# Performance work log

Measured on AMD Instinct MI355X. Metric: run time of the kernel, lower is better.

The kernel has to match this reference:

```python
import jax, jax.numpy as jnp
import numpy as np

HEADS = 16
DIM_HEAD = 64
QUERY_DIM = 1024
INNER_DIM = HEADS * DIM_HEAD  # 1024
SCALE = DIM_HEAD ** (-0.5)


def setup_inputs() -> dict:
    key = jax.random.key(0)
    ks = jax.random.split(key, 6)
    B, S = 4, 2048
    hidden_states = jax.random.normal(ks[0], (B, S, QUERY_DIM), dtype=jnp.float32)
    # Linear weights stored as [in, out] for x @ W convention
    init = 1.0 / np.sqrt(QUERY_DIM)
    Wq = jax.random.uniform(ks[1], (QUERY_DIM, INNER_DIM), jnp.float32, -init, init)
    Wk = jax.random.uniform(ks[2], (QUERY_DIM, INNER_DIM), jnp.float32, -init, init)
    Wv = jax.random.uniform(ks[3], (QUERY_DIM, INNER_DIM), jnp.float32, -init, init)
    Wo = jax.random.uniform(ks[4], (INNER_DIM, QUERY_DIM), jnp.float32, -init, init)
    bo = jax.random.uniform(ks[5], (QUERY_DIM,), jnp.float32, -init, init)
    return {"hidden_states": hidden_states, "Wq": Wq, "Wk": Wk, "Wv": Wv, "Wo": Wo, "bo": bo}


def reference(hidden_states, Wq, Wk, Wv, Wo, bo):
    B, S, _ = hidden_states.shape
    # Projections
    q = hidden_states @ Wq  # [B,S,inner]
    k = hidden_states @ Wk
    v = hidden_states @ Wv
    # [B, H, S, D]
    q = q.reshape(B, S, HEADS, DIM_HEAD).transpose(0, 2, 1, 3)
    k = k.reshape(B, S, HEADS, DIM_HEAD).transpose(0, 2, 1, 3)
    v = v.reshape(B, S, HEADS, DIM_HEAD).transpose(0, 2, 1, 3)
    # Attention scores and softmax (scale after matmul, as in source)
    scores = jnp.einsum('bhqd,bhkd->bhqk', q, k) * SCALE
    attn = jax.nn.softmax(scores, axis=-1)
    out = jnp.einsum('bhqk,bhkd->bhqd', attn, v)  # [B,H,S,D]
    out = out.transpose(0, 2, 1, 3).reshape(B, S, INNER_DIM)
    return out @ Wo + bo
```

## Files before the change

### kernel.cpp

```cpp
#include <hip/hip_runtime.h>
#include <stdint.h>

typedef short v8s __attribute__((ext_vector_type(8)));
typedef float v4f __attribute__((ext_vector_type(4)));
typedef unsigned int u32;
typedef unsigned short us;

#define LOG2E 1.44269504088896340736f

__device__ __forceinline__ u32 f2u(float x) {
  union { float f; u32 u; } t; t.f = x; return t.u;
}

__device__ __forceinline__ unsigned short bfr(float x) {
  u32 u = f2u(x);
  u32 r = u + 0x7FFFu + ((u >> 16) & 1u);
  return (unsigned short)(r >> 16);
}

__device__ __forceinline__ u32 pk2(float a, float b) {
  return __builtin_amdgcn_perm(f2u(b) + 0x8000u, f2u(a) + 0x8000u, 0x07060302u);
}

__device__ __forceinline__ void async16(const void* g, void* l) {
  __builtin_amdgcn_global_load_lds(
      (const __attribute__((address_space(1))) u32*)g,
      (__attribute__((address_space(3))) u32*)l, 16, 0, 0);
}

#define MFMA_K32(A, B, C) __builtin_amdgcn_mfma_f32_16x16x32_bf16((A), (B), (C), 0, 0, 0)

__global__ void cast_h_kernel(const float4* __restrict__ in, ushort4* __restrict__ out, int n4) {
  int i = blockIdx.x * blockDim.x + threadIdx.x;
  if (i < n4) {
    float4 v = in[i];
    ushort4 o;
    o.x = bfr(v.x); o.y = bfr(v.y); o.z = bfr(v.z); o.w = bfr(v.w);
    out[i] = o;
  }
}

__global__ void transpose_cast4_kernel(const float* __restrict__ W0, const float* __restrict__ W1,
                                       const float* __restrict__ W2, const float* __restrict__ W3,
                                       us* __restrict__ O0, us* __restrict__ O1,
                                       us* __restrict__ O2, us* __restrict__ O3) {
  __shared__ float tile[32][33];
  const int z = blockIdx.z;
  const float* in = (z == 0) ? W0 : (z == 1) ? W1 : (z == 2) ? W2 : W3;
  us* out = (z == 0) ? O0 : (z == 1) ? O1 : (z == 2) ? O2 : O3;
  const float scale = (z == 0) ? 0.125f * LOG2E : 1.0f;
  const int N = 1024;
  int n0 = blockIdx.x * 32, k0 = blockIdx.y * 32;
  int tx = threadIdx.x, ty = threadIdx.y;
#pragma unroll
  for (int j = 0; j < 32; j += 8)
    tile[ty + j][tx] = in[(size_t)(k0 + ty + j) * N + n0 + tx];
  __syncthreads();
#pragma unroll
  for (int j = 0; j < 32; j += 8)
    out[(size_t)(n0 + ty + j) * 1024 + k0 + tx] = bfr(tile[tx][ty + j] * scale);
}

template <int MODE>
__global__ __launch_bounds__(256)
void gemm_bt_kernel(const us* __restrict__ A, const us* __restrict__ Bt,
                    us* __restrict__ dQ, us* __restrict__ dK, us* __restrict__ dV,
                    float* __restrict__ outF, const float* __restrict__ bias) {
  __shared__ __align__(16) us sm[MODE == 3 ? 16896 : 16384];
  us* As = sm;
  us* Bs = sm + 8192;
  const int tid = threadIdx.x;
  const int wid = tid >> 6;
  const int lane = tid & 63;
  const int quad = lane >> 4;
  const int l16 = lane & 15;
  const int tile_m = blockIdx.y * 128;
  const int tile_n = blockIdx.x * 128;
  const bool vpath = (MODE == 3) && (tile_n >= 2048);

  const int srow = wid * 32 + (lane >> 3);
  const int sc = lane & 7;

  v4f zero = {0.f, 0.f, 0.f, 0.f};
  v4f acc[4][4];
#pragma unroll
  for (int i = 0; i < 4; ++i)
#pragma unroll
    for (int j = 0; j < 4; ++j) acc[i][j] = zero;

  const int wm = (wid >> 1) * 64;
  const int wn = (wid & 1) * 64;

  for (int k0 = 0; k0 < 1024; k0 += 64) {
#pragma unroll
    for (int it = 0; it < 4; ++it) {
      int rr = srow + it * 8;
      int cg = sc ^ (rr & 7);
      async16(A + (size_t)(tile_m + rr) * 1024 + k0 + cg * 8, &As[rr * 64 + sc * 8]);
      async16(Bt + (size_t)(tile_n + rr) * 1024 + k0 + cg * 8, &Bs[rr * 64 + sc * 8]);
    }
    __syncthreads();
#pragma unroll
    for (int ks = 0; ks < 2; ++ks) {
      v8s a[4], b[4];
#pragma unroll
      for (int i = 0; i < 4; ++i) {
        int row = wm + i * 16 + l16;
        a[i] = *(const v8s*)&As[row * 64 + (((ks * 4 + quad) ^ (row & 7)) * 8)];
      }
#pragma unroll
      for (int j = 0; j < 4; ++j) {
        int row = wn + j * 16 + l16;
        b[j] = *(const v8s*)&Bs[row * 64 + (((ks * 4 + quad) ^ (row & 7)) * 8)];
      }
      if (vpath) {
#pragma unroll
        for (int i = 0; i < 4; ++i)
#pragma unroll
          for (int j = 0; j < 4; ++j)
            acc[i][j] = MFMA_K32(a[i], b[j], acc[i][j]);
      } else {
#pragma unroll
        for (int i = 0; i < 4; ++i)
#pragma unroll
          for (int j = 0; j < 4; ++j)
            acc[i][j] = MFMA_K32(b[j], a[i], acc[i][j]);
      }
    }
    __syncthreads();
  }

  if (MODE == 2) {
#pragma unroll
    for (int i = 0; i < 4; ++i) {
      int row = tile_m + wm + i * 16 + l16;
#pragma unroll
      for (int j = 0; j < 4; ++j) {
        int col = tile_n + wn + j * 16 + quad * 4;
        float4 bv = *(const float4*)&bias[col];
        float4 o;
        o.x = acc[i][j][0] + bv.x; o.y = acc[i][j][1] + bv.y;
        o.z = acc[i][j][2] + bv.z; o.w = acc[i][j][3] + bv.w;
        *(float4*)&outF[(size_t)row * 1024 + col] = o;
      }
    }
  } else if (!vpath) {
    us* base = (tile_n < 1024) ? dQ : dK;
    const int coln = tile_n & 1023;
#pragma unroll
    for (int i = 0; i < 4; ++i) {
      int row = tile_m + wm + i * 16 + l16;
      int b_ = row >> 11, s_ = row & 2047;
#pragma unroll
      for (int j = 0; j < 4; ++j) {
        int col = coln + wn + j * 16 + quad * 4;
        int h = (col >> 6) & 15, d = col & 63;
        uint2 pk = make_uint2(pk2(acc[i][j][0], acc[i][j][1]), pk2(acc[i][j][2], acc[i][j][3]));
        *(uint2*)&base[((size_t)(b_ * 16 + h) * 2048 + s_) * 64 + d] = pk;
      }
    }
  } else {
    const int vn = tile_n - 2048;
#pragma unroll
    for (int i = 0; i < 4; ++i) {
      int sp = wm + (i >> 1) * 32 + quad * 8 + (i & 1) * 4;
#pragma unroll
      for (int j = 0; j < 4; ++j) {
        int col = wn + j * 16 + l16;
        uint2 pk = make_uint2(pk2(acc[i][j][0], acc[i][j][1]), pk2(acc[i][j][2], acc[i][j][3]));
        *(uint2*)&sm[col * 132 + sp] = pk;
      }
    }
    __syncthreads();
    const int b_ = tile_m >> 11;
    const int sbase = tile_m & 2047;
#pragma unroll
    for (int it = 0; it < 8; ++it) {
      int u = it * 256 + tid;
      int col = u >> 4, sp = (u & 15) * 8;
      v8s val = *(const v8s*)&sm[col * 132 + sp];
      int colg = vn + col;
      int h = (colg >> 6) & 15, d = colg & 63;
      *(v8s*)&dV[((size_t)(b_ * 16 + h) * 64 + d) * 2048 + sbase + sp] = val;
    }
  }
}

__global__ __launch_bounds__(256, 2)
void flash_kernel(const us* __restrict__ Q, const us* __restrict__ K,
                  const us* __restrict__ Vt, us* __restrict__ O) {
  __shared__ __align__(16) us sm[16384];
  us* Ks = sm;
  us* Vts = sm + 8192;

  const int tid = threadIdx.x;
  const int wid = tid >> 6;
  const int lane = tid & 63;
  const int quad = lane >> 4;
  const int l16 = lane & 15;
  const int id = blockIdx.x;
  const int bh = id & 63;
  const int q0 = (id >> 6) * 256;
  const int wq = wid * 64;
  const us* Qp = Q + (size_t)bh * (2048 * 64);
  const us* Kp = K + (size_t)bh * (2048 * 64);
  const us* Vp = Vt + (size_t)bh * (64 * 2048);

  v8s qB[4][2];
#pragma unroll
  for (int mi = 0; mi < 4; ++mi)
#pragma unroll
    for (int ks = 0; ks < 2; ++ks)
      qB[mi][ks] = *(const v8s*)&Qp[(size_t)(q0 + wq + mi * 16 + l16) * 64 + ks * 32 + quad * 8];

  v4f zero = {0.f, 0.f, 0.f, 0.f};
  v4f o[4][4];
#pragma unroll
  for (int i = 0; i < 4; ++i)
#pragma unroll
    for (int mi = 0; mi < 4; ++mi) o[i][mi] = zero;
  v4f l_acc[4] = {zero, zero, zero, zero};
  const us one_bf = 0x3F80;
  const v8s ones = {(short)one_bf, (short)one_bf, (short)one_bf, (short)one_bf,
                    (short)one_bf, (short)one_bf, (short)one_bf, (short)one_bf};

  for (int kv0 = 0; kv0 < 2048; kv0 += 128) {
    __syncthreads();
    {
      int r0 = wid * 32 + (lane >> 3);
      int c = lane & 7;
#pragma unroll
      for (int it = 0; it < 4; ++it) {
        int rr = r0 + it * 8;
        int cg = c ^ (rr & 7);
        async16(Kp + (size_t)(kv0 + rr) * 64 + cg * 8, &Ks[rr * 64 + c * 8]);
      }
    }
    {
      int d0 = wid * 16 + (lane >> 4);
      int c = lane & 15;
#pragma unroll
      for (int it = 0; it < 4; ++it) {
        int dd = d0 + it * 4;
        int cg = c ^ (dd & 15);
        async16(Vp + (size_t)dd * 2048 + kv0 + cg * 8, &Vts[dd * 128 + c * 8]);
      }
    }
    __syncthreads();

#pragma unroll
    for (int hf = 0; hf < 2; ++hf) {
      v4f sT[4][4];
#pragma unroll
      for (int m = 0; m < 4; ++m)
#pragma unroll
        for (int mi = 0; mi < 4; ++mi) sT[m][mi] = zero;
#pragma unroll
      for (int ks = 0; ks < 2; ++ks) {
        v8s kA[4];
#pragma unroll
        for (int m = 0; m < 4; ++m) {
          int kvr = hf * 64 + m * 16 + l16;
          int cc = (ks * 4 + quad) ^ (l16 & 7);
          kA[m] = *(const v8s*)&Ks[kvr * 64 + cc * 8];
        }
#pragma unroll
        for (int m = 0; m < 4; ++m)
#pragma unroll
          for (int mi = 0; mi < 4; ++mi)
            sT[m][mi] = MFMA_K32(kA[m], qB[mi][ks], sT[m][mi]);
      }

#pragma unroll
      for (int cp = 0; cp < 2; ++cp) {
        v8s bp[4];
#pragma unroll
        for (int mi = 0; mi < 4; ++mi) {
          union { u32 w[4]; v8s s; } u;
#pragma unroll
          for (int dm = 0; dm < 2; ++dm) {
            int m = cp * 2 + dm;
            float p0 = __builtin_amdgcn_exp2f(sT[m][mi][0]);
            float p1 = __builtin_amdgcn_exp2f(sT[m][mi][1]);
            float p2 = __builtin_amdgcn_exp2f(sT[m][mi][2]);
            float p3 = __builtin_amdgcn_exp2f(sT[m][mi][3]);
            u.w[dm * 2] = pk2(p0, p1);
            u.w[dm * 2 + 1] = pk2(p2, p3);
          }
          bp[mi] = u.s;
          l_acc[mi] = MFMA_K32(ones, bp[mi], l_acc[mi]);
        }
#pragma unroll
        for (int i = 0; i < 4; ++i) {
          int d = i * 16 + l16;
          int cc = (hf * 8 + cp * 4 + quad) ^ (d & 15);
          v8s vt = *(const v8s*)&Vts[d * 128 + cc * 8];
#pragma unroll
          for (int mi = 0; mi < 4; ++mi)
            o[i][mi] = MFMA_K32(vt, bp[mi], o[i][mi]);
        }
      }
    }
  }

  float invl[4];
#pragma unroll
  for (int mi = 0; mi < 4; ++mi) invl[mi] = 1.0f / l_acc[mi][0];

  __syncthreads();
#pragma unroll
  for (int mi = 0; mi < 4; ++mi) {
    int q = wq + mi * 16 + l16;
#pragma unroll
    for (int i = 0; i < 4; ++i)
#pragma unroll
      for (int rp = 0; rp < 4; rp += 2) {
        int d = i * 16 + quad * 4 + rp;
        u32 pk = pk2(o[i][mi][rp] * invl[mi], o[i][mi][rp + 1] * invl[mi]);
        *(u32*)&sm[q * 64 + ((d >> 3) ^ (q & 7)) * 8 + (d & 7)] = pk;
      }
  }
  __syncthreads();
  const int b_ = bh >> 4, h_ = bh & 15;
#pragma unroll
  for (int it = 0; it < 8; ++it) {
    int u = it * 256 + tid;
    int row = u >> 3, ch = u & 7;
    v8s val = *(const v8s*)&sm[row * 64 + (ch ^ (row & 7)) * 8];
    *(v8s*)&O[((size_t)(b_ * 2048 + q0 + row)) * 1024 + h_ * 64 + ch * 8] = val;
  }
}

extern "C" void kernel_launch(void* const* d_in, const int* in_sizes, int n_in,
                              void* d_out, int out_size, void* d_ws, size_t ws_size,
                              hipStream_t stream) {
  const float* Hs = (const float*)d_in[0];
  const float* Wq = (const float*)d_in[1];
  const float* Wk = (const float*)d_in[2];
  const float* Wv = (const float*)d_in[3];
  const float* Wo = (const float*)d_in[4];
  const float* bo = (const float*)d_in[5];
  float* out = (float*)d_out;
  char* ws = (char*)d_ws;
  const size_t MiB = 1ull << 20;
  us* Hb  = (us*)(ws);
  us* Wqt = (us*)(ws + 16 * MiB);
  us* Wkt = (us*)(ws + 18 * MiB);
  us* Wvt = (us*)(ws + 20 * MiB);
  us* Wot = (us*)(ws + 22 * MiB);
  us* Qb  = (us*)(ws + 24 * MiB);
  us* Kb  = (us*)(ws + 40 * MiB);
  us* Vtb = (us*)(ws + 56 * MiB);
  us* Ob  = Hb;
  (void)Wkt; (void)Wvt;

  cast_h_kernel<<<8192, 256, 0, stream>>>((const float4*)Hs, (ushort4*)Hb, 2097152);
  transpose_cast4_kernel<<<dim3(32, 32, 4), dim3(32, 8), 0, stream>>>(Wq, Wk, Wv, Wo,
                                                                      Wqt, Wkt, Wvt, Wot);
  gemm_bt_kernel<3><<<dim3(24, 64), 256, 0, stream>>>(Hb, Wqt, Qb, Kb, Vtb, nullptr, nullptr);
  flash_kernel<<<512, 256, 0, stream>>>(Qb, Kb, Vtb, Ob);
  gemm_bt_kernel<2><<<dim3(8, 64), 256, 0, stream>>>(Ob, Wot, nullptr, nullptr, nullptr, out, bo);
}
```

Before: 256.0 us.

## Triple-buffer GEMM with async prefetch, 128x256 tiles, and MFMA priority hints

Rewrites the projection GEMM to use 512-thread blocks with 128x256 output tiles. A three-stage LDS ring is fed by async global-to-LDS loads issued two k-steps ahead, with vmcnt waits replacing the double __syncthreads per iteration. It also raises wave priority around MFMA blocks in both the GEMM and the flash attention kernel. The goal is to hide global load latency and improve B-tile reuse, at the cost of 144KB LDS per block (limiting occupancy) and fewer blocks for the small output GEMM (256 blocks).

```diff
diff --git a/kernel.cpp b/kernel.cpp
--- a/kernel.cpp
+++ b/kernel.cpp
@@ -62,24 +62,44 @@
 }
 
 template <int MODE>
-__global__ __launch_bounds__(256)
-void gemm_bt_kernel(const us* __restrict__ A, const us* __restrict__ Bt,
-                    us* __restrict__ dQ, us* __restrict__ dK, us* __restrict__ dV,
-                    float* __restrict__ outF, const float* __restrict__ bias) {
-  __shared__ __align__(16) us sm[MODE == 3 ? 16896 : 16384];
-  us* As = sm;
-  us* Bs = sm + 8192;
+__global__ __launch_bounds__(512, 2)
+void gemm3_kernel(const us* __restrict__ A, const us* __restrict__ Bt,
+                  us* __restrict__ dQ, us* __restrict__ dK, us* __restrict__ dV,
+                  float* __restrict__ outF, const float* __restrict__ bias) {
+  __shared__ __align__(16) us sm[73728];
+  us* const AsB = sm;
+  us* const BsB = sm + 3 * 8192;
+
   const int tid = threadIdx.x;
   const int wid = tid >> 6;
   const int lane = tid & 63;
   const int quad = lane >> 4;
   const int l16 = lane & 15;
   const int tile_m = blockIdx.y * 128;
-  const int tile_n = blockIdx.x * 128;
+  const int tile_n = blockIdx.x * 256;
   const bool vpath = (MODE == 3) && (tile_n >= 2048);
 
-  const int srow = wid * 32 + (lane >> 3);
-  const int sc = lane & 7;
+  const int srow = tid >> 3;
+  const int sc = tid & 7;
+  const int scg = sc ^ (srow & 7);
+
+  const us* const GA = A + (size_t)(tile_m + srow) * 1024 + scg * 8;
+  const us* const GB = Bt + (size_t)(tile_n + srow) * 1024 + scg * 8;
+  us* const LA = AsB + srow * 64 + sc * 8;
+  us* const LB = BsB + srow * 64 + sc * 8;
+
+  auto ISSUE = [&](int j, int b) {
+    const us* ga = GA + j * 64;
+    us* la = LA + b * 8192;
+#pragma unroll
+    for (int it = 0; it < 2; ++it)
+      async16(ga + it * 64 * 1024, la + it * 64 * 64);
+    const us* gb = GB + j * 64;
+    us* lb = LB + b * 16384;
+#pragma unroll
+    for (int it = 0; it < 4; ++it)
+      async16(gb + it * 64 * 1024, lb + it * 64 * 64);
+  };
 
   v4f zero = {0.f, 0.f, 0.f, 0.f};
   v4f acc[4][4];
@@ -88,18 +108,30 @@
 #pragma unroll
     for (int j = 0; j < 4; ++j) acc[i][j] = zero;
 
-  const int wm = (wid >> 1) * 64;
-  const int wn = (wid & 1) * 64;
-
-  for (int k0 = 0; k0 < 1024; k0 += 64) {
-#pragma unroll
-    for (int it = 0; it < 4; ++it) {
-      int rr = srow + it * 8;
-      int cg = sc ^ (rr & 7);
-      async16(A + (size_t)(tile_m + rr) * 1024 + k0 + cg * 8, &As[rr * 64 + sc * 8]);
-      async16(Bt + (size_t)(tile_n + rr) * 1024 + k0 + cg * 8, &Bs[rr * 64 + sc * 8]);
-    }
-    __syncthreads();
+  const int wm = (wid >> 2) * 64;
+  const int wn = (wid & 3) * 64;
+
+  ISSUE(0, 0);
+  ISSUE(1, 1);
+
+  int bt = 0;
+#pragma unroll 1
+  for (int t = 0; t < 16; ++t) {
+    if (t < 15)
+      asm volatile("s_waitcnt vmcnt(6)" ::: "memory");
+    else
+      asm volatile("s_waitcnt vmcnt(0)" ::: "memory");
+    __builtin_amdgcn_s_barrier();
+    asm volatile("" ::: "memory");
+
+    if (t + 2 < 16) {
+      int b2 = bt + 2;
+      if (b2 >= 3) b2 -= 3;
+      ISSUE(t + 2, b2);
+    }
+
+    const us* As = AsB + bt * 8192;
+    const us* Bs = BsB + bt * 16384;
 #pragma unroll
     for (int ks = 0; ks < 2; ++ks) {
       v8s a[4], b[4];
@@ -113,6 +145,7 @@
         int row = wn + j * 16 + l16;
         b[j] = *(const v8s*)&Bs[row * 64 + (((ks * 4 + quad) ^ (row & 7)) * 8)];
       }
+      __builtin_amdgcn_s_setprio(1);
       if (vpath) {
 #pragma unroll
         for (int i = 0; i < 4; ++i)
@@ -126,8 +159,9 @@
           for (int j = 0; j < 4; ++j)
             acc[i][j] = MFMA_K32(b[j], a[i], acc[i][j]);
       }
-    }
-    __syncthreads();
+      __builtin_amdgcn_s_setprio(0);
+    }
+    if (++bt >= 3) bt = 0;
   }
 
   if (MODE == 2) {
@@ -160,6 +194,7 @@
       }
     }
   } else {
+    __syncthreads();
     const int vn = tile_n - 2048;
 #pragma unroll
     for (int i = 0; i < 4; ++i) {
@@ -176,7 +211,7 @@
     const int sbase = tile_m & 2047;
 #pragma unroll
     for (int it = 0; it < 8; ++it) {
-      int u = it * 256 + tid;
+      int u = it * 512 + tid;
       int col = u >> 4, sp = (u & 15) * 8;
       v8s val = *(const v8s*)&sm[col * 132 + sp];
       int colg = vn + col;
@@ -264,11 +299,13 @@
           int cc = (ks * 4 + quad) ^ (l16 & 7);
           kA[m] = *(const v8s*)&Ks[kvr * 64 + cc * 8];
         }
+        __builtin_amdgcn_s_setprio(1);
 #pragma unroll
         for (int m = 0; m < 4; ++m)
 #pragma unroll
           for (int mi = 0; mi < 4; ++mi)
             sT[m][mi] = MFMA_K32(kA[m], qB[mi][ks], sT[m][mi]);
+        __builtin_amdgcn_s_setprio(0);
       }
 
 #pragma unroll
@@ -290,6 +327,7 @@
           bp[mi] = u.s;
           l_acc[mi] = MFMA_K32(ones, bp[mi], l_acc[mi]);
         }
+        __builtin_amdgcn_s_setprio(1);
 #pragma unroll
         for (int i = 0; i < 4; ++i) {
           int d = i * 16 + l16;
@@ -299,6 +337,7 @@
           for (int mi = 0; mi < 4; ++mi)
             o[i][mi] = MFMA_K32(vt, bp[mi], o[i][mi]);
         }
+        __builtin_amdgcn_s_setprio(0);
       }
     }
   }
@@ -357,7 +396,7 @@
   cast_h_kernel<<<8192, 256, 0, stream>>>((const float4*)Hs, (ushort4*)Hb, 2097152);
   transpose_cast4_kernel<<<dim3(32, 32, 4), dim3(32, 8), 0, stream>>>(Wq, Wk, Wv, Wo,
                                                                       Wqt, Wkt, Wvt, Wot);
-  gemm_bt_kernel<3><<<dim3(24, 64), 256, 0, stream>>>(Hb, Wqt, Qb, Kb, Vtb, nullptr, nullptr);
+  gemm3_kernel<3><<<dim3(12, 64), 512, 0, stream>>>(Hb, Wqt, Qb, Kb, Vtb, nullptr, nullptr);
   flash_kernel<<<512, 256, 0, stream>>>(Qb, Kb, Vtb, Ob);
-  gemm_bt_kernel<2><<<dim3(8, 64), 256, 0, stream>>>(Ob, Wot, nullptr, nullptr, nullptr, out, bo);
-}
+  gemm3_kernel<2><<<dim3(4, 64), 512, 0, stream>>>(Ob, Wot, nullptr, nullptr, nullptr, out, bo);
+}
```

Result: no change. 251.2 us (-1.9%).
